# Performance work log

Measured on AMD Instinct MI355X. Metric: run time of the kernel, lower is better.

The kernel has to match this reference:

```python
import jax, jax.numpy as jnp
import numpy as np

N = 1024          # n_nodes
F = 32            # n_input_features (per-node embedding dim)
HID = 64          # n_hidden_features
OUT = 32          # n_output_features


def setup_inputs() -> dict:
    key = jax.random.key(0)
    k = jax.random.split(key, 7)
    Edges = jax.random.uniform(k[0], (N, N), dtype=jnp.float32)
    Coordinates = jax.random.normal(k[1], (N, 3), dtype=jnp.float32)
    Embeddings = jax.random.normal(k[2], (N, F), dtype=jnp.float32)
    # nn.Linear params: W (out, in), b (out,)
    s1 = 1.0 / np.sqrt(2 * F)
    s2 = 1.0 / np.sqrt(HID)
    W1 = jax.random.uniform(k[3], (HID, 2 * F), dtype=jnp.float32, minval=-s1, maxval=s1)
    b1 = jax.random.uniform(k[4], (HID,), dtype=jnp.float32, minval=-s1, maxval=s1)
    W2 = jax.random.uniform(k[5], (OUT, HID), dtype=jnp.float32, minval=-s2, maxval=s2)
    b2 = jax.random.uniform(k[6], (OUT,), dtype=jnp.float32, minval=-s2, maxval=s2)
    return {"Edges": Edges, "Coordinates": Coordinates, "Embeddings": Embeddings,
            "W1": W1, "b1": b1, "W2": W2, "b2": b2}


def _swish(x):
    return x * jax.nn.sigmoid(x)


def reference(Edges, Coordinates, Embeddings, W1, b1, W2, b2):
    # pairwise euclidean distances (torch.cdist p=2), grad-safe on the zero diagonal
    diff = Coordinates[:, None, :] - Coordinates[None, :, :]          # (N, N, 3)
    sq = jnp.sum(diff * diff, axis=-1)                                # (N, N)
    dist = jnp.where(sq > 0, jnp.sqrt(jnp.where(sq > 0, sq, 1.0)), 0.0)
    w = Edges * dist                                                  # (N, N)

    # H[i, j] = concat(Emb[i], Emb[j]); first Linear applied without
    # materializing the (N, N, 2F) tensor:
    # (w * [h_i, h_j]) @ W1^T = w * (h_i @ W1[:, :F]^T + h_j @ W1[:, F:]^T)
    A = Embeddings @ W1[:, :F].T                                      # (N, HID) from h_i half
    B = Embeddings @ W1[:, F:].T                                      # (N, HID) from h_j half
    pre1 = w[:, :, None] * (A[:, None, :] + B[None, :, :]) + b1       # (N, N, HID)
    h1 = _swish(pre1)
    pre2 = jnp.einsum('ijh,oh->ijo', h1, W2) + b2                     # (N, N, OUT)
    return _swish(pre2)                                               # squeeze() is a no-op (OUT > 1)
```

## Files before the change

kernel.cpp:

```cpp
#include <hip/hip_runtime.h>
#include <math.h>

#define NN   1024
#define FF   32
#define HID  64
#define OUTF 32
#define ITER 8

typedef unsigned int  uint;
typedef unsigned short ushort;
typedef _Float16 halfx8  __attribute__((ext_vector_type(8)));
typedef __fp16   fp16x2  __attribute__((ext_vector_type(2)));
typedef float    floatx16 __attribute__((ext_vector_type(16)));

#define WS_A    0
#define WS_B    (WS_A + NN*HID)
#define WS_C4   (WS_B + NN*HID)
#define WS_B1   (WS_C4 + NN*4)
#define WS_B2   (WS_B1 + HID)
#define WS_W2H  (WS_B2 + 64)

__device__ __forceinline__ float swish(float x) {
    float e = __builtin_amdgcn_exp2f(x * -1.442695040888963f);
    return x * __builtin_amdgcn_rcpf(1.0f + e);
}

__global__ void prep_kernel(
    const float* __restrict__ Coords,
    const float* __restrict__ Emb,
    const float* __restrict__ W1,
    const float* __restrict__ b1,
    const float* __restrict__ W2,
    const float* __restrict__ b2,
    float* __restrict__ ws)
{
    const int b = blockIdx.x;
    const int t = threadIdx.x;
    if (b < NN) {
        float accA = 0.f, accB = 0.f;
        const float* w1row = W1 + t * (2 * FF);
        const float* erow  = Emb + b * FF;
        #pragma unroll
        for (int f = 0; f < FF; ++f) {
            float e = erow[f];
            accA = fmaf(e, w1row[f],      accA);
            accB = fmaf(e, w1row[FF + f], accB);
        }
        ws[WS_A + b * HID + t] = accA;
        ws[WS_B + b * HID + t] = accB;
    } else {
        if (t < HID)  ws[WS_B1 + t] = b1[t];
        if (t < OUTF) ws[WS_B2 + t] = b2[t];
        #pragma unroll 1
        for (int n = t; n < NN; n += 64) {
            ws[WS_C4 + n * 4 + 0] = Coords[n * 3 + 0];
            ws[WS_C4 + n * 4 + 1] = Coords[n * 3 + 1];
            ws[WS_C4 + n * 4 + 2] = Coords[n * 3 + 2];
            ws[WS_C4 + n * 4 + 3] = 0.f;
        }
        ushort* w2h = (ushort*)(ws + WS_W2H);
        const int n  = t & 31;
        const int kh = (t >> 5) * 8;
        #pragma unroll
        for (int c = 0; c < 4; ++c) {
            #pragma unroll
            for (int j = 0; j < 8; ++j) {
                const int k = c * 16 + kh + j;
                union { _Float16 h; ushort u; } cv;
                cv.h = (_Float16)W2[n * HID + k];
                w2h[(c * 64 + t) * 8 + j] = cv.u;
            }
        }
    }
}

__global__ __launch_bounds__(256, 4) void main_kernel(
    const float* __restrict__ Edges,
    const float* __restrict__ ws,
    float* __restrict__ out)
{
    __shared__ float lds[ITER * HID + HID + ITER * 4];

    const int t    = threadIdx.x;
    const int lane = t & 63;
    const int wave = t >> 6;
    const int j0   = blockIdx.x * 128 + wave * 32;
    const int i0   = blockIdx.y * ITER;
    const int p    = lane & 31;
    const int half = lane >> 5;
    const int jp   = j0 + p;

    {
        const float* srcA = ws + WS_A + (size_t)i0 * HID;
        if (t < 128) {
            *(float4*)&lds[t * 4] = *(const float4*)(srcA + t * 4);
        } else if (t < 144) {
            *(float4*)&lds[ITER * HID + (t - 128) * 4] =
                *(const float4*)(ws + WS_B1 + (t - 128) * 4);
        } else if (t < 152) {
            *(float4*)&lds[ITER * HID + HID + (t - 144) * 4] =
                *(const float4*)(ws + WS_C4 + (size_t)(i0 + (t - 144)) * 4);
        }
    }

    const ushort* w2hp = (const ushort*)(ws + WS_W2H);
    halfx8 bh[4];
    #pragma unroll
    for (int c = 0; c < 4; ++c)
        bh[c] = *(const halfx8*)(w2hp + (c * 64 + lane) * 8);

    const float* __restrict__ Bj = ws + WS_B + (size_t)jp * HID;
    float bv[4][8];
    #pragma unroll
    for (int c = 0; c < 4; ++c) {
        const int h0 = c * 16 + half * 8;
        *(float4*)(&bv[c][0]) = *(const float4*)(Bj + h0);
        *(float4*)(&bv[c][4]) = *(const float4*)(Bj + h0 + 4);
    }
    const float4 cj  = *(const float4*)(ws + WS_C4 + (size_t)jp * 4);
    const float  b2n = ws[WS_B2 + p];

    __syncthreads();

    const float* egp = Edges + (size_t)i0 * NN + jp;
    float eg = *egp;

    #pragma unroll 1
    for (int it = 0; it < ITER; ++it) {
        const int i = i0 + it;
        const float eg_cur = eg;
        if (it + 1 < ITER) eg = egp[(size_t)(it + 1) * NN];

        const float4 civ = *(const float4*)&lds[ITER * HID + HID + it * 4];
        const float dx = civ.x - cj.x, dy = civ.y - cj.y, dz = civ.z - cj.z;
        const float dist = sqrtf(dx * dx + dy * dy + dz * dz);
        const float w = eg_cur * dist;

        union FragH { fp16x2 h2[4]; halfx8 v; } ah[4];
        #pragma unroll
        for (int c = 0; c < 4; ++c) {
            const int ho = c * 16 + half * 8;
            float av[8], b1c[8];
            *(float4*)(av + 0)  = *(const float4*)&lds[it * HID + ho];
            *(float4*)(av + 4)  = *(const float4*)&lds[it * HID + ho + 4];
            *(float4*)(b1c + 0) = *(const float4*)&lds[ITER * HID + ho];
            *(float4*)(b1c + 4) = *(const float4*)&lds[ITER * HID + ho + 4];
            #pragma unroll
            for (int jj = 0; jj < 8; jj += 2) {
                const float p0 = fmaf(w, av[jj]     + bv[c][jj],     b1c[jj]);
                const float p1 = fmaf(w, av[jj + 1] + bv[c][jj + 1], b1c[jj + 1]);
                ah[c].h2[jj >> 1] = __builtin_amdgcn_cvt_pkrtz(swish(p0), swish(p1));
            }
        }

        floatx16 acc = {0.f,0.f,0.f,0.f,0.f,0.f,0.f,0.f,
                        0.f,0.f,0.f,0.f,0.f,0.f,0.f,0.f};
        #pragma unroll
        for (int c = 0; c < 4; ++c)
            acc = __builtin_amdgcn_mfma_f32_32x32x16_f16(ah[c].v, bh[c], acc, 0, 0, 0);

        float* __restrict__ ob = out + ((size_t)i * NN + j0) * OUTF + p;
        #pragma unroll
        for (int r = 0; r < 16; ++r) {
            const int m = (r & 3) + 8 * (r >> 2) + 4 * half;
            __builtin_nontemporal_store(swish(acc[r] + b2n), ob + m * OUTF);
        }
    }
}

extern "C" void kernel_launch(void* const* d_in, const int* in_sizes, int n_in,
                              void* d_out, int out_size, void* d_ws, size_t ws_size,
                              hipStream_t stream)
{
    const float* Edges  = (const float*)d_in[0];
    const float* Coords = (const float*)d_in[1];
    const float* Emb    = (const float*)d_in[2];
    const float* W1     = (const float*)d_in[3];
    const float* b1     = (const float*)d_in[4];
    const float* W2     = (const float*)d_in[5];
    const float* b2     = (const float*)d_in[6];
    float* ws  = (float*)d_ws;
    float* out = (float*)d_out;

    hipLaunchKernelGGL(prep_kernel, dim3(NN + 1), dim3(64), 0, stream,
                       Coords, Emb, W1, b1, W2, b2, ws);
    hipLaunchKernelGGL(main_kernel, dim3(NN / 128, NN / ITER), dim3(256), 0, stream,
                       Edges, ws, out);
}
```

Baseline: 170.9 us.

## Fuse prep into main kernel and swap MFMA operands for vectorized stores

Drops the separate prep kernel and computes the per-node A/B projections, the fp16 W2 fragments, the biases and the coordinates inside each block of the main kernel, so one launch and the workspace round-trip go away. The MFMA operand order is swapped so each lane holds four contiguous output features, which lets the epilogue write float4 nontemporal stores instead of scalar strided ones. The MFMA is also issued per chunk, interleaved with the swish computation. In exchange every block recomputes the B projection for its 32 j columns (a 64x32 dot product per lane) and the A rows, which adds redundant ALU work and repeated W1 reads from cache.

```diff
diff --git a/kernel.cpp b/kernel.cpp
--- a/kernel.cpp
+++ b/kernel.cpp
@@ -12,74 +12,27 @@
 typedef _Float16 halfx8  __attribute__((ext_vector_type(8)));
 typedef __fp16   fp16x2  __attribute__((ext_vector_type(2)));
 typedef float    floatx16 __attribute__((ext_vector_type(16)));
-
-#define WS_A    0
-#define WS_B    (WS_A + NN*HID)
-#define WS_C4   (WS_B + NN*HID)
-#define WS_B1   (WS_C4 + NN*4)
-#define WS_B2   (WS_B1 + HID)
-#define WS_W2H  (WS_B2 + 64)
+typedef float    floatx4  __attribute__((ext_vector_type(4)));
 
 __device__ __forceinline__ float swish(float x) {
     float e = __builtin_amdgcn_exp2f(x * -1.442695040888963f);
     return x * __builtin_amdgcn_rcpf(1.0f + e);
 }
 
-__global__ void prep_kernel(
+__global__ __launch_bounds__(256, 4) void fused_kernel(
+    const float* __restrict__ Edges,
     const float* __restrict__ Coords,
     const float* __restrict__ Emb,
     const float* __restrict__ W1,
     const float* __restrict__ b1,
     const float* __restrict__ W2,
     const float* __restrict__ b2,
-    float* __restrict__ ws)
-{
-    const int b = blockIdx.x;
-    const int t = threadIdx.x;
-    if (b < NN) {
-        float accA = 0.f, accB = 0.f;
-        const float* w1row = W1 + t * (2 * FF);
-        const float* erow  = Emb + b * FF;
-        #pragma unroll
-        for (int f = 0; f < FF; ++f) {
-            float e = erow[f];
-            accA = fmaf(e, w1row[f],      accA);
-            accB = fmaf(e, w1row[FF + f], accB);
-        }
-        ws[WS_A + b * HID + t] = accA;
-        ws[WS_B + b * HID + t] = accB;
-    } else {
-        if (t < HID)  ws[WS_B1 + t] = b1[t];
-        if (t < OUTF) ws[WS_B2 + t] = b2[t];
-        #pragma unroll 1
-        for (int n = t; n < NN; n += 64) {
-            ws[WS_C4 + n * 4 + 0] = Coords[n * 3 + 0];
-            ws[WS_C4 + n * 4 + 1] = Coords[n * 3 + 1];
-            ws[WS_C4 + n * 4 + 2] = Coords[n * 3 + 2];
-            ws[WS_C4 + n * 4 + 3] = 0.f;
-        }
-        ushort* w2h = (ushort*)(ws + WS_W2H);
-        const int n  = t & 31;
-        const int kh = (t >> 5) * 8;
-        #pragma unroll
-        for (int c = 0; c < 4; ++c) {
-            #pragma unroll
-            for (int j = 0; j < 8; ++j) {
-                const int k = c * 16 + kh + j;
-                union { _Float16 h; ushort u; } cv;
-                cv.h = (_Float16)W2[n * HID + k];
-                w2h[(c * 64 + t) * 8 + j] = cv.u;
-            }
-        }
-    }
-}
-
-__global__ __launch_bounds__(256, 4) void main_kernel(
-    const float* __restrict__ Edges,
-    const float* __restrict__ ws,
     float* __restrict__ out)
 {
-    __shared__ float lds[ITER * HID + HID + ITER * 4];
+    __shared__ float lA[ITER * HID];
+    __shared__ float lb1[HID];
+    __shared__ float lb2[OUTF];
+    __shared__ float lci[ITER * 4];
 
     const int t    = threadIdx.x;
     const int lane = t & 63;
@@ -91,34 +44,81 @@
     const int jp   = j0 + p;
 
     {
-        const float* srcA = ws + WS_A + (size_t)i0 * HID;
-        if (t < 128) {
-            *(float4*)&lds[t * 4] = *(const float4*)(srcA + t * 4);
-        } else if (t < 144) {
-            *(float4*)&lds[ITER * HID + (t - 128) * 4] =
-                *(const float4*)(ws + WS_B1 + (t - 128) * 4);
-        } else if (t < 152) {
-            *(float4*)&lds[ITER * HID + HID + (t - 144) * 4] =
-                *(const float4*)(ws + WS_C4 + (size_t)(i0 + (t - 144)) * 4);
+        const int r = t >> 5;
+        const int h = t & 31;
+        const float* er = Emb + (size_t)(i0 + r) * FF;
+        float ef[FF];
+        #pragma unroll
+        for (int f4 = 0; f4 < FF / 4; ++f4)
+            *(float4*)(ef + f4 * 4) = ((const float4*)er)[f4];
+        const float* w0 = W1 + (size_t)h * (2 * FF);
+        const float* w1r = W1 + (size_t)(h + 32) * (2 * FF);
+        float a0 = 0.f, a1 = 0.f;
+        #pragma unroll
+        for (int f4 = 0; f4 < FF / 4; ++f4) {
+            const float4 q0 = ((const float4*)w0)[f4];
+            const float4 q1 = ((const float4*)w1r)[f4];
+            a0 = fmaf(ef[f4*4+0], q0.x, fmaf(ef[f4*4+1], q0.y,
+                 fmaf(ef[f4*4+2], q0.z, fmaf(ef[f4*4+3], q0.w, a0))));
+            a1 = fmaf(ef[f4*4+0], q1.x, fmaf(ef[f4*4+1], q1.y,
+                 fmaf(ef[f4*4+2], q1.z, fmaf(ef[f4*4+3], q1.w, a1))));
+        }
+        lA[r * HID + h]      = a0;
+        lA[r * HID + h + 32] = a1;
+    }
+    if (t < HID / 4) {
+        *(float4*)&lb1[t * 4] = ((const float4*)b1)[t];
+    } else if (t < HID / 4 + OUTF / 4) {
+        const int q = t - HID / 4;
+        *(float4*)&lb2[q * 4] = ((const float4*)b2)[q];
+    }
+    if (t < ITER) {
+        lci[t * 4 + 0] = Coords[(i0 + t) * 3 + 0];
+        lci[t * 4 + 1] = Coords[(i0 + t) * 3 + 1];
+        lci[t * 4 + 2] = Coords[(i0 + t) * 3 + 2];
+        lci[t * 4 + 3] = 0.f;
+    }
+
+    union FragW { _Float16 h[8]; halfx8 v; } bhu[4];
+    {
+        const float* w2r = W2 + (size_t)p * HID;
+        #pragma unroll
+        for (int c = 0; c < 4; ++c) {
+            const int k0 = c * 16 + half * 8;
+            float wv[8];
+            *(float4*)(wv + 0) = *(const float4*)(w2r + k0);
+            *(float4*)(wv + 4) = *(const float4*)(w2r + k0 + 4);
+            #pragma unroll
+            for (int j = 0; j < 8; ++j) bhu[c].h[j] = (_Float16)wv[j];
         }
     }
-
-    const ushort* w2hp = (const ushort*)(ws + WS_W2H);
-    halfx8 bh[4];
-    #pragma unroll
-    for (int c = 0; c < 4; ++c)
-        bh[c] = *(const halfx8*)(w2hp + (c * 64 + lane) * 8);
-
-    const float* __restrict__ Bj = ws + WS_B + (size_t)jp * HID;
     float bv[4][8];
-    #pragma unroll
-    for (int c = 0; c < 4; ++c) {
-        const int h0 = c * 16 + half * 8;
-        *(float4*)(&bv[c][0]) = *(const float4*)(Bj + h0);
-        *(float4*)(&bv[c][4]) = *(const float4*)(Bj + h0 + 4);
+    {
+        const float* ej = Emb + (size_t)jp * FF;
+        float ef[FF];
+        #pragma unroll
+        for (int f4 = 0; f4 < FF / 4; ++f4)
+            *(float4*)(ef + f4 * 4) = ((const float4*)ej)[f4];
+        #pragma unroll
+        for (int c = 0; c < 4; ++c) {
+            #pragma unroll
+            for (int jj = 0; jj < 8; ++jj) {
+                const int h = c * 16 + half * 8 + jj;
+                const float* wr = W1 + (size_t)h * (2 * FF) + FF;
+                float acc = 0.f;
+                #pragma unroll
+                for (int f4 = 0; f4 < FF / 4; ++f4) {
+                    const float4 wq = ((const float4*)wr)[f4];
+                    acc = fmaf(ef[f4*4+0], wq.x, fmaf(ef[f4*4+1], wq.y,
+                          fmaf(ef[f4*4+2], wq.z, fmaf(ef[f4*4+3], wq.w, acc))));
+                }
+                bv[c][jj] = acc;
+            }
+        }
     }
-    const float4 cj  = *(const float4*)(ws + WS_C4 + (size_t)jp * 4);
-    const float  b2n = ws[WS_B2 + p];
+    const float cjx = Coords[jp * 3 + 0];
+    const float cjy = Coords[jp * 3 + 1];
+    const float cjz = Coords[jp * 3 + 2];
 
     __syncthreads();
 
@@ -131,39 +131,41 @@
         const float eg_cur = eg;
         if (it + 1 < ITER) eg = egp[(size_t)(it + 1) * NN];
 
-        const float4 civ = *(const float4*)&lds[ITER * HID + HID + it * 4];
-        const float dx = civ.x - cj.x, dy = civ.y - cj.y, dz = civ.z - cj.z;
+        const float4 civ = *(const float4*)&lci[it * 4];
+        const float dx = civ.x - cjx, dy = civ.y - cjy, dz = civ.z - cjz;
         const float dist = sqrtf(dx * dx + dy * dy + dz * dz);
         const float w = eg_cur * dist;
 
-        union FragH { fp16x2 h2[4]; halfx8 v; } ah[4];
+        floatx16 acc = {0.f,0.f,0.f,0.f,0.f,0.f,0.f,0.f,
+                        0.f,0.f,0.f,0.f,0.f,0.f,0.f,0.f};
         #pragma unroll
         for (int c = 0; c < 4; ++c) {
             const int ho = c * 16 + half * 8;
             float av[8], b1c[8];
-            *(float4*)(av + 0)  = *(const float4*)&lds[it * HID + ho];
-            *(float4*)(av + 4)  = *(const float4*)&lds[it * HID + ho + 4];
-            *(float4*)(b1c + 0) = *(const float4*)&lds[ITER * HID + ho];
-            *(float4*)(b1c + 4) = *(const float4*)&lds[ITER * HID + ho + 4];
+            *(float4*)(av + 0)  = *(const float4*)&lA[it * HID + ho];
+            *(float4*)(av + 4)  = *(const float4*)&lA[it * HID + ho + 4];
+            *(float4*)(b1c + 0) = *(const float4*)&lb1[ho];
+            *(float4*)(b1c + 4) = *(const float4*)&lb1[ho + 4];
+            union FragH { fp16x2 h2[4]; halfx8 v; } ah;
             #pragma unroll
             for (int jj = 0; jj < 8; jj += 2) {
                 const float p0 = fmaf(w, av[jj]     + bv[c][jj],     b1c[jj]);
                 const float p1 = fmaf(w, av[jj + 1] + bv[c][jj + 1], b1c[jj + 1]);
-                ah[c].h2[jj >> 1] = __builtin_amdgcn_cvt_pkrtz(swish(p0), swish(p1));
+                ah.h2[jj >> 1] = __builtin_amdgcn_cvt_pkrtz(swish(p0), swish(p1));
             }
+            acc = __builtin_amdgcn_mfma_f32_32x32x16_f16(bhu[c].v, ah.v, acc, 0, 0, 0);
         }
 
-        floatx16 acc = {0.f,0.f,0.f,0.f,0.f,0.f,0.f,0.f,
-                        0.f,0.f,0.f,0.f,0.f,0.f,0.f,0.f};
+        float* __restrict__ ob = out + ((size_t)i * NN + jp) * OUTF;
         #pragma unroll
-        for (int c = 0; c < 4; ++c)
-            acc = __builtin_amdgcn_mfma_f32_32x32x16_f16(ah[c].v, bh[c], acc, 0, 0, 0);
-
-        float* __restrict__ ob = out + ((size_t)i * NN + j0) * OUTF + p;
-        #pragma unroll
-        for (int r = 0; r < 16; ++r) {
-            const int m = (r & 3) + 8 * (r >> 2) + 4 * half;
-            __builtin_nontemporal_store(swish(acc[r] + b2n), ob + m * OUTF);
+        for (int q = 0; q < 4; ++q) {
+            const float4 bb = *(const float4*)&lb2[q * 8 + half * 4];
+            floatx4 v;
+            v.x = swish(acc[q * 4 + 0] + bb.x);
+            v.y = swish(acc[q * 4 + 1] + bb.y);
+            v.z = swish(acc[q * 4 + 2] + bb.z);
+            v.w = swish(acc[q * 4 + 3] + bb.w);
+            __builtin_nontemporal_store(v, (floatx4*)(ob + q * 8 + half * 4));
         }
     }
 }
@@ -179,11 +181,9 @@
     const float* b1     = (const float*)d_in[4];
     const float* W2     = (const float*)d_in[5];
     const float* b2     = (const float*)d_in[6];
-    float* ws  = (float*)d_ws;
     float* out = (float*)d_out;
+    (void)d_ws; (void)ws_size;
 
-    hipLaunchKernelGGL(prep_kernel, dim3(NN + 1), dim3(64), 0, stream,
-                       Coords, Emb, W1, b1, W2, b2, ws);
-    hipLaunchKernelGGL(main_kernel, dim3(NN / 128, NN / ITER), dim3(256), 0, stream,
-                       Edges, ws, out);
+    hipLaunchKernelGGL(fused_kernel, dim3(NN / 128, NN / ITER), dim3(256), 0, stream,
+                       Edges, Coords, Emb, W1, b1, W2, b2, out);
 }
```

Result: slower. 289.9 us (+69.7%).
